# Kernel optimization log

Measured on AMD Instinct MI355X. Metric: run time of the kernel, lower is better.

## Reference

```python
import jax, jax.numpy as jnp
import numpy as np

B, S, D = 8, 1024, 1024   # batch, routed-over rows, feature dim (input_dim)
E = 1024                  # output_dim (== S so gather indices are in range)
K = 2                     # top-k
ALPHA = 0.01


def setup_inputs() -> dict:
    key = jax.random.key(0)
    kx, kw = jax.random.split(key)
    x = jax.random.normal(kx, (B, S, D), dtype=jnp.float32)
    # nn.Linear(input_dim, output_dim, bias=False) weight: [E, D]
    W = jax.random.normal(kw, (E, D), dtype=jnp.float32) / np.sqrt(D).astype(np.float32)
    return {"x": x, "W": W}


def reference(x, W):
    # logits = proj(x): [B, S, E]  (temperature == 1.0 -> no scaling)
    logits = jnp.einsum('bsd,ed->bse', x, W)
    probs = jax.nn.softmax(logits, axis=-1)
    topk_probs, topk_idx = jax.lax.top_k(probs, K)            # [B, S, K]
    # router_selections: gather rows of x along dim 1 -> [B, S, K, D]
    sel = x[jnp.arange(B)[:, None, None], topk_idx]
    # y = sum_k topk_probs * selected rows -> [B, S, D]
    y = jnp.einsum('bsk,bskd->bsd', topk_probs, sel)
    # auxiliary load-balance loss
    router_probs = probs.mean(axis=(0, 1))                    # [E]
    counts = jnp.bincount(topk_idx.reshape(-1), length=E).astype(probs.dtype)
    router_fraction = counts / counts.sum()
    aux_loss = ALPHA * E * jnp.sum(router_probs * router_fraction)
    return y, aux_loss
```

## Files before the change

kernel.cpp:

```cpp
#include <hip/hip_runtime.h>

#define MTOK 8192
#define ED   1024

typedef short s16x8 __attribute__((ext_vector_type(8)));
typedef float f32x4 __attribute__((ext_vector_type(4)));
typedef int   i32x4 __attribute__((ext_vector_type(4)));
typedef unsigned short u16x4 __attribute__((ext_vector_type(4)));

__device__ __forceinline__ unsigned short f2bf(float f) {
    unsigned u = __builtin_bit_cast(unsigned, f);
    u += 0x7fff + ((u >> 16) & 1);
    return (unsigned short)(u >> 16);
}
__device__ __forceinline__ float bf2f(unsigned short h) {
    unsigned u = ((unsigned)h) << 16;
    return __builtin_bit_cast(float, u);
}

__global__ __launch_bounds__(256) void split_bf16_kernel(
        const float* __restrict__ src, unsigned short* __restrict__ hi,
        unsigned short* __restrict__ lo, int* __restrict__ counts, int n4) {
    if (blockIdx.x == 0) {
#pragma unroll
        for (int i = 0; i < 4; ++i) counts[threadIdx.x + i * 256] = 0;
    }
    int idx = blockIdx.x * 256 + threadIdx.x;
    const int stride = gridDim.x * 256;
    for (; idx < n4; idx += stride) {
        float4 v = ((const float4*)src)[idx];
        u16x4 h, l;
        h[0] = f2bf(v.x); l[0] = f2bf(v.x - bf2f(h[0]));
        h[1] = f2bf(v.y); l[1] = f2bf(v.y - bf2f(h[1]));
        h[2] = f2bf(v.z); l[2] = f2bf(v.z - bf2f(h[2]));
        h[3] = f2bf(v.w); l[3] = f2bf(v.w - bf2f(h[3]));
        ((u16x4*)hi)[idx] = h;
        ((u16x4*)lo)[idx] = l;
    }
}

__device__ __forceinline__ void gload16(const void* g, void* l) {
    __builtin_amdgcn_global_load_lds(
        (const __attribute__((address_space(1))) void*)g,
        (__attribute__((address_space(3))) void*)l, 16, 0, 0);
}

__device__ __forceinline__ int cvtpk(float a, float b) {
    int r;
    asm("v_cvt_pk_bf16_f32 %0, %1, %2" : "=v"(r) : "v"(a), "v"(b));
    return r;
}

__device__ __forceinline__ void cvt_write(void* dstHi, void* dstLo,
                                          const float4 f0, const float4 f1) {
    i32x4 h, l;
    h[0] = cvtpk(f0.x, f0.y); h[1] = cvtpk(f0.z, f0.w);
    h[2] = cvtpk(f1.x, f1.y); h[3] = cvtpk(f1.z, f1.w);
    l[0] = cvtpk(f0.x - __builtin_bit_cast(float, h[0] << 16),
                 f0.y - __builtin_bit_cast(float, h[0] & 0xffff0000));
    l[1] = cvtpk(f0.z - __builtin_bit_cast(float, h[1] << 16),
                 f0.w - __builtin_bit_cast(float, h[1] & 0xffff0000));
    l[2] = cvtpk(f1.x - __builtin_bit_cast(float, h[2] << 16),
                 f1.y - __builtin_bit_cast(float, h[2] & 0xffff0000));
    l[3] = cvtpk(f1.z - __builtin_bit_cast(float, h[3] << 16),
                 f1.w - __builtin_bit_cast(float, h[3] & 0xffff0000));
    *(i32x4*)dstHi = h;
    *(i32x4*)dstLo = l;
}

__global__ __launch_bounds__(256, 2) void gemm_mfma_split_kernel(
        const float* __restrict__ Xf,
        const unsigned short* __restrict__ Whi, const unsigned short* __restrict__ Wlo,
        float* __restrict__ C) {
    __shared__ __align__(16) unsigned char smem[2 * 32768];

    const int bid = blockIdx.x;
    const int xcd = bid & 7;
    const int j   = bid >> 3;
    const int bm  = xcd * 8 + (j >> 3);
    const int bn  = j & 7;

    const int tid  = threadIdx.x;
    const int lane = tid & 63;
    const int wid  = tid >> 6;

    const int srow = lane >> 2;
    const int sg   = (lane & 3) ^ ((lane >> 3) & 3);
    const float* gA = Xf + (size_t)(bm * 128 + wid * 32 + srow) * ED + sg * 8;
    const unsigned short* gB = ((wid < 2) ? Whi : Wlo)
            + (size_t)(bn * 128 + (wid & 1) * 64 + srow) * ED + sg * 8;
    unsigned char* const dB = smem + 16384 + ((wid < 2) ? 0 : 8192) + (wid & 1) * 4096;

    float4 fA0, fA1, fA2, fA3;

#define ALOAD(kk)                                                    \
    fA0 = *(const float4*)(gA + (kk));                               \
    fA1 = *(const float4*)(gA + (kk) + 4);                           \
    fA2 = *(const float4*)(gA + (kk) + 16 * 1024);                   \
    fA3 = *(const float4*)(gA + (kk) + 16 * 1024 + 4);

#define BSTAGE(buf, kk)                                              \
    _Pragma("unroll")                                                \
    for (int c = 0; c < 4; ++c)                                      \
        gload16(gB + (kk) + c * (16 * ED), dB + (buf) * 32768 + c * 1024);

#define AWRITE(buf)                                                              \
    cvt_write(smem + (buf) * 32768 + (2 * wid) * 1024 + lane * 16,               \
              smem + (buf) * 32768 + 8192 + (2 * wid) * 1024 + lane * 16,        \
              fA0, fA1);                                                         \
    cvt_write(smem + (buf) * 32768 + (2 * wid + 1) * 1024 + lane * 16,           \
              smem + (buf) * 32768 + 8192 + (2 * wid + 1) * 1024 + lane * 16,    \
              fA2, fA3);

    const int wm = wid >> 1, wn = wid & 1;
    const int fr = lane & 15, fg = lane >> 4;
    const int pg = fg ^ ((fr >> 1) & 3);
    const int aoff = (wm * 64 + fr) * 32 + pg * 8;
    const int boff = (wn * 64 + fr) * 32 + pg * 8;

    f32x4 acc[4][4] = {};

    ALOAD(0);
    BSTAGE(0, 0);
    AWRITE(0);
    asm volatile("s_waitcnt vmcnt(0) lgkmcnt(0)" ::: "memory");
    __builtin_amdgcn_s_barrier();

    for (int t = 0; t < 32; ++t) {
        const int cur = t & 1;
        if (t < 31) { ALOAD((t + 1) * 32); BSTAGE(cur ^ 1, (t + 1) * 32); }

        const unsigned short* Ah = (const unsigned short*)(smem + cur * 32768);
        const unsigned short* Al = Ah + 4096;
        const unsigned short* Bh = Ah + 8192;
        const unsigned short* Bl = Ah + 12288;

        s16x8 ah[4], al[4], bh[4], bl[4];
#pragma unroll
        for (int i = 0; i < 4; ++i) {
            ah[i] = *(const s16x8*)&Ah[aoff + i * 512];
            al[i] = *(const s16x8*)&Al[aoff + i * 512];
            bh[i] = *(const s16x8*)&Bh[boff + i * 512];
            bl[i] = *(const s16x8*)&Bl[boff + i * 512];
        }
#pragma unroll
        for (int i = 0; i < 4; ++i)
#pragma unroll
            for (int jj = 0; jj < 4; ++jj) {
                acc[i][jj] = __builtin_amdgcn_mfma_f32_16x16x32_bf16(ah[i], bh[jj], acc[i][jj], 0, 0, 0);
                acc[i][jj] = __builtin_amdgcn_mfma_f32_16x16x32_bf16(ah[i], bl[jj], acc[i][jj], 0, 0, 0);
                acc[i][jj] = __builtin_amdgcn_mfma_f32_16x16x32_bf16(al[i], bh[jj], acc[i][jj], 0, 0, 0);
            }

        if (t < 31) AWRITE(cur ^ 1);

        asm volatile("s_waitcnt vmcnt(0) lgkmcnt(0)" ::: "memory");
        __builtin_amdgcn_s_barrier();
    }
#undef ALOAD
#undef BSTAGE
#undef AWRITE

    const int crow = bm * 128 + wm * 64 + fg * 4;
    const int ccol = bn * 128 + wn * 64 + fr;
#pragma unroll
    for (int i = 0; i < 4; ++i)
#pragma unroll
        for (int jj = 0; jj < 4; ++jj)
#pragma unroll
            for (int r = 0; r < 4; ++r)
                C[(size_t)(crow + i * 16 + r) * ED + ccol + jj * 16] = acc[i][jj][r];
}

#define BM 128
#define BN 128
#define BK 32
#define LDA (BM + 4)
#define LDB (BN + 4)

__global__ __launch_bounds__(256) void gemm_logits_kernel(const float* __restrict__ X,
                                                          const float* __restrict__ W,
                                                          float* __restrict__ C) {
    __shared__ float As[BK][LDA];
    __shared__ float Bs[BK][LDB];
    const int bm  = blockIdx.y * BM;
    const int bn  = blockIdx.x * BN;
    const int tid = threadIdx.x;
    const int tx  = tid & 15;
    const int ty  = tid >> 4;
    const int lr  = tid >> 3;
    const int lc  = (tid & 7) << 2;

    float acc[8][8];
#pragma unroll
    for (int i = 0; i < 8; ++i)
#pragma unroll
        for (int j = 0; j < 8; ++j) acc[i][j] = 0.f;

    for (int k0 = 0; k0 < ED; k0 += BK) {
#pragma unroll
        for (int i = 0; i < 4; ++i) {
            const int r = lr + i * 32;
            float4 va = *(const float4*)&X[(size_t)(bm + r) * ED + k0 + lc];
            As[lc + 0][r] = va.x; As[lc + 1][r] = va.y;
            As[lc + 2][r] = va.z; As[lc + 3][r] = va.w;
            float4 vb = *(const float4*)&W[(size_t)(bn + r) * ED + k0 + lc];
            Bs[lc + 0][r] = vb.x; Bs[lc + 1][r] = vb.y;
            Bs[lc + 2][r] = vb.z; Bs[lc + 3][r] = vb.w;
        }
        __syncthreads();
#pragma unroll
        for (int kk = 0; kk < BK; ++kk) {
            float a[8], b[8];
            *(float4*)&a[0] = *(const float4*)&As[kk][ty * 8];
            *(float4*)&a[4] = *(const float4*)&As[kk][ty * 8 + 4];
            *(float4*)&b[0] = *(const float4*)&Bs[kk][tx * 8];
            *(float4*)&b[4] = *(const float4*)&Bs[kk][tx * 8 + 4];
#pragma unroll
            for (int i = 0; i < 8; ++i)
#pragma unroll
                for (int j = 0; j < 8; ++j)
                    acc[i][j] = fmaf(a[i], b[j], acc[i][j]);
        }
        __syncthreads();
    }
#pragma unroll
    for (int i = 0; i < 8; ++i) {
        const int r = bm + ty * 8 + i;
        float4* dst = (float4*)&C[(size_t)r * ED + bn + tx * 8];
        dst[0] = make_float4(acc[i][0], acc[i][1], acc[i][2], acc[i][3]);
        dst[1] = make_float4(acc[i][4], acc[i][5], acc[i][6], acc[i][7]);
    }
}

__device__ __forceinline__ bool better(float v, int i, float bv, int bi) {
    return (v > bv) || (v == bv && i < bi);
}

__global__ __launch_bounds__(256, 8) void softmax_wave_kernel(
        const float* __restrict__ X, float* __restrict__ OUT,
        float* __restrict__ partial, int* __restrict__ counts) {
    __shared__ float L[4 * 1024];
    const int tid  = threadIdx.x;
    const int lane = tid & 63;
    const int w    = tid >> 6;
    const int t    = blockIdx.x * 4 + w;

    const float4* row4 = (const float4*)&OUT[(size_t)t * ED];
    float4 p[4];
#pragma unroll
    for (int i = 0; i < 4; ++i) p[i] = row4[lane + 64 * i];

    float v1 = -1e30f, v2 = -1e30f; int i1 = 0x7fffffff, i2 = 0x7fffffff;
#pragma unroll
    for (int i = 0; i < 4; ++i) {
        const float vv[4] = {p[i].x, p[i].y, p[i].z, p[i].w};
#pragma unroll
        for (int c = 0; c < 4; ++c) {
            const int e = 256 * i + 4 * lane + c;
            const float v = vv[c];
            if (better(v, e, v1, i1)) { v2 = v1; i2 = i1; v1 = v; i1 = e; }
            else if (better(v, e, v2, i2)) { v2 = v; i2 = e; }
        }
    }
#pragma unroll
    for (int off = 32; off; off >>= 1) {
        const float ov1 = __shfl_xor(v1, off); const int oi1 = __shfl_xor(i1, off);
        const float ov2 = __shfl_xor(v2, off); const int oi2 = __shfl_xor(i2, off);
        if (better(ov1, oi1, v1, i1)) {
            float nv2; int ni2;
            if (better(v1, i1, ov2, oi2)) { nv2 = v1; ni2 = i1; }
            else { nv2 = ov2; ni2 = oi2; }
            v1 = ov1; i1 = oi1; v2 = nv2; i2 = ni2;
        } else if (better(ov1, oi1, v2, i2)) { v2 = ov1; i2 = oi1; }
    }
    const float m = v1;

    float s = 0.f;
#pragma unroll
    for (int i = 0; i < 4; ++i) {
        p[i].x = __expf(p[i].x - m); p[i].y = __expf(p[i].y - m);
        p[i].z = __expf(p[i].z - m); p[i].w = __expf(p[i].w - m);
        s += p[i].x + p[i].y + p[i].z + p[i].w;
    }
#pragma unroll
    for (int off = 32; off; off >>= 1) s += __shfl_xor(s, off);
    const float inv = 1.f / s;

#pragma unroll
    for (int i = 0; i < 4; ++i) {
        float4 q = make_float4(p[i].x * inv, p[i].y * inv, p[i].z * inv, p[i].w * inv);
        *(float4*)&L[w * 1024 + i * 256 + lane * 4] = q;
    }

    const float p1 = inv;
    const float p2 = __expf(v2 - m) * inv;
    const int b = t >> 10;
    const float4* x1 = (const float4*)&X[((size_t)(b << 10) + i1) * ED];
    const float4* x2 = (const float4*)&X[((size_t)(b << 10) + i2) * ED];
    float4* yrow = (float4*)&OUT[(size_t)t * ED];
#pragma unroll
    for (int i = 0; i < 4; ++i) {
        const int idx = lane + 64 * i;
        const float4 a = x1[idx];
        const float4 c = x2[idx];
        float4 r;
        r.x = fmaf(p1, a.x, p2 * c.x);
        r.y = fmaf(p1, a.y, p2 * c.y);
        r.z = fmaf(p1, a.z, p2 * c.z);
        r.w = fmaf(p1, a.w, p2 * c.w);
        yrow[idx] = r;
    }

    if (lane == 0) { atomicAdd(&counts[i1], 1); atomicAdd(&counts[i2], 1); }

    __syncthreads();
    float4 s0 = *(float4*)&L[0 * 1024 + tid * 4];
    float4 s1 = *(float4*)&L[1 * 1024 + tid * 4];
    float4 s2 = *(float4*)&L[2 * 1024 + tid * 4];
    float4 s3 = *(float4*)&L[3 * 1024 + tid * 4];
    float4 r;
    r.x = (s0.x + s1.x) + (s2.x + s3.x);
    r.y = (s0.y + s1.y) + (s2.y + s3.y);
    r.z = (s0.z + s1.z) + (s2.z + s3.z);
    r.w = (s0.w + s1.w) + (s2.w + s3.w);
    *(float4*)&partial[(size_t)blockIdx.x * 1024 + tid * 4] = r;
}

__global__ __launch_bounds__(256) void aux1_kernel(const float* __restrict__ partial,
                                                   const int* __restrict__ counts,
                                                   float* __restrict__ dotPartial) {
    __shared__ float red[16][16];
    const int tid = threadIdx.x;
    const int el  = tid & 15;
    const int ch  = tid >> 4;
    const int e   = blockIdx.x * 16 + el;
    float s = 0.f;
    for (int k = 0; k < 128; ++k)
        s += partial[(size_t)(ch * 128 + k) * 1024 + e];
    red[ch][el] = s;
    __syncthreads();
    if (tid < 16) {
        float rs = 0.f;
#pragma unroll
        for (int c = 0; c < 16; ++c) rs += red[c][tid];
        float val = rs * (float)counts[blockIdx.x * 16 + tid];
#pragma unroll
        for (int off = 8; off; off >>= 1) val += __shfl_xor(val, off);
        if (tid == 0) dotPartial[blockIdx.x] = val;
    }
}

__global__ void aux2_kernel(const float* __restrict__ dotPartial, float* __restrict__ out) {
    const int lane = threadIdx.x;
    float v = dotPartial[lane];
#pragma unroll
    for (int off = 32; off; off >>= 1) v += __shfl_xor(v, off);
    if (lane == 0)
        out[(size_t)MTOK * ED] = v * (0.01f * 1024.f / (8192.f * 16384.f));
}

#define TOKS_PER_BLK 16
__global__ __launch_bounds__(256) void softmax_topk_y_kernel(
        const float* __restrict__ X, float* __restrict__ OUT,
        float* __restrict__ router_sum, int* __restrict__ counts) {
    __shared__ float routerLocal[ED];
    __shared__ float redMax[4];
    __shared__ float redSum[4];
    __shared__ float wV1[4]; __shared__ int wI1[4];
    __shared__ float wV2[4]; __shared__ int wI2[4];

    const int tid  = threadIdx.x;
    const int lane = tid & 63;
    const int wave = tid >> 6;

    for (int e = tid; e < ED; e += 256) routerLocal[e] = 0.f;
    __syncthreads();

    const int t0 = blockIdx.x * TOKS_PER_BLK;
    for (int t = t0; t < t0 + TOKS_PER_BLK; ++t) {
        const float* lrow = &OUT[(size_t)t * ED];
        float l[4];
#pragma unroll
        for (int i = 0; i < 4; ++i) l[i] = lrow[tid + i * 256];

        float m = fmaxf(fmaxf(l[0], l[1]), fmaxf(l[2], l[3]));
#pragma unroll
        for (int off = 32; off; off >>= 1) m = fmaxf(m, __shfl_xor(m, off));
        if (lane == 0) redMax[wave] = m;
        __syncthreads();
        m = fmaxf(fmaxf(redMax[0], redMax[1]), fmaxf(redMax[2], redMax[3]));

        float p[4]; float s = 0.f;
#pragma unroll
        for (int i = 0; i < 4; ++i) { p[i] = expf(l[i] - m); s += p[i]; }
#pragma unroll
        for (int off = 32; off; off >>= 1) s += __shfl_xor(s, off);
        if (lane == 0) redSum[wave] = s;

        float v1 = -1e30f, v2 = -1e30f; int i1 = 0x7fffffff, i2 = 0x7fffffff;
#pragma unroll
        for (int i = 0; i < 4; ++i) {
            const float v = l[i]; const int ix = tid + i * 256;
            if (better(v, ix, v1, i1)) { v2 = v1; i2 = i1; v1 = v; i1 = ix; }
            else if (better(v, ix, v2, i2)) { v2 = v; i2 = ix; }
        }
#pragma unroll
        for (int off = 32; off; off >>= 1) {
            const float ov1 = __shfl_xor(v1, off); const int oi1 = __shfl_xor(i1, off);
            const float ov2 = __shfl_xor(v2, off); const int oi2 = __shfl_xor(i2, off);
            if (better(ov1, oi1, v1, i1)) {
                float nv2; int ni2;
                if (better(v1, i1, ov2, oi2)) { nv2 = v1; ni2 = i1; }
                else { nv2 = ov2; ni2 = oi2; }
                v1 = ov1; i1 = oi1; v2 = nv2; i2 = ni2;
            } else if (better(ov1, oi1, v2, i2)) { v2 = ov1; i2 = oi1; }
        }
        if (lane == 0) { wV1[wave] = v1; wI1[wave] = i1; wV2[wave] = v2; wI2[wave] = i2; }
        __syncthreads();

        v1 = wV1[0]; i1 = wI1[0]; v2 = wV2[0]; i2 = wI2[0];
#pragma unroll
        for (int w = 1; w < 4; ++w) {
            const float ov1 = wV1[w]; const int oi1 = wI1[w];
            const float ov2 = wV2[w]; const int oi2 = wI2[w];
            if (better(ov1, oi1, v1, i1)) {
                float nv2; int ni2;
                if (better(v1, i1, ov2, oi2)) { nv2 = v1; ni2 = i1; }
                else { nv2 = ov2; ni2 = oi2; }
                v1 = ov1; i1 = oi1; v2 = nv2; i2 = ni2;
            } else if (better(ov1, oi1, v2, i2)) { v2 = ov1; i2 = oi1; }
        }
        const float stot = redSum[0] + redSum[1] + redSum[2] + redSum[3];
        const float inv = 1.f / stot;

#pragma unroll
        for (int i = 0; i < 4; ++i) routerLocal[tid + i * 256] += p[i] * inv;

        const float p1 = expf(v1 - m) * inv;
        const float p2 = expf(v2 - m) * inv;

        const int b = t >> 10;
        const float4* x1 = (const float4*)&X[((size_t)(b << 10) + i1) * ED];
        const float4* x2 = (const float4*)&X[((size_t)(b << 10) + i2) * ED];
        float4* yrow = (float4*)&OUT[(size_t)t * ED];
        const float4 a = x1[tid];
        const float4 c = x2[tid];
        float4 r;
        r.x = fmaf(p1, a.x, p2 * c.x);
        r.y = fmaf(p1, a.y, p2 * c.y);
        r.z = fmaf(p1, a.z, p2 * c.z);
        r.w = fmaf(p1, a.w, p2 * c.w);
        yrow[tid] = r;

        if (tid == 0) { atomicAdd(&counts[i1], 1); atomicAdd(&counts[i2], 1); }
        __syncthreads();
    }

    for (int e = tid; e < ED; e += 256) atomicAdd(&router_sum[e], routerLocal[e]);
}

__global__ __launch_bounds__(256) void aux_kernel(const float* __restrict__ router_sum,
                                                  const int* __restrict__ counts,
                                                  float* __restrict__ out) {
    __shared__ float red[4];
    const int tid = threadIdx.x;
    float s = 0.f;
    for (int e = tid; e < ED; e += 256)
        s += (router_sum[e] * (1.f / 8192.f)) * ((float)counts[e] * (1.f / 16384.f));
#pragma unroll
    for (int off = 32; off; off >>= 1) s += __shfl_xor(s, off);
    if ((tid & 63) == 0) red[tid >> 6] = s;
    __syncthreads();
    if (tid == 0) out[(size_t)MTOK * ED] = 0.01f * 1024.f * (red[0] + red[1] + red[2] + red[3]);
}

extern "C" void kernel_launch(void* const* d_in, const int* in_sizes, int n_in,
                              void* d_out, int out_size, void* d_ws, size_t ws_size,
                              hipStream_t stream) {
    const float* X = (const float*)d_in[0];
    const float* W = (const float*)d_in[1];
    float* out = (float*)d_out;

    const size_t WS_NEED = (size_t)ED * ED * 2 * sizeof(unsigned short)
                         + (size_t)2048 * 1024 * sizeof(float)
                         + 64 * sizeof(float) + ED * sizeof(int);

    if (ws_size >= WS_NEED) {
        unsigned short* Whi = (unsigned short*)d_ws;
        unsigned short* Wlo = Whi + (size_t)ED * ED;
        float* partial      = (float*)(Wlo + (size_t)ED * ED);
        float* dotPartial   = partial + (size_t)2048 * 1024;
        int*   counts       = (int*)(dotPartial + 64);

        split_bf16_kernel<<<512, 256, 0, stream>>>(W, Whi, Wlo, counts, ED * ED / 4);
        gemm_mfma_split_kernel<<<512, 256, 0, stream>>>(X, Whi, Wlo, out);
        softmax_wave_kernel<<<MTOK / 4, 256, 0, stream>>>(X, out, partial, counts);
        aux1_kernel<<<64, 256, 0, stream>>>(partial, counts, dotPartial);
        aux2_kernel<<<1, 64, 0, stream>>>(dotPartial, out);
    } else {
        float* router_sum = (float*)d_ws;
        int*   counts     = (int*)((char*)d_ws + ED * sizeof(float));
        hipMemsetAsync(d_ws, 0, ED * (sizeof(float) + sizeof(int)), stream);
        dim3 ggrid(ED / BN, MTOK / BM);
        gemm_logits_kernel<<<ggrid, 256, 0, stream>>>(X, W, out);
        softmax_topk_y_kernel<<<MTOK / TOKS_PER_BLK, 256, 0, stream>>>(X, out, router_sum, counts);
        aux_kernel<<<1, 256, 0, stream>>>(router_sum, counts, out);
    }
}
```

Before: 90.69 us.

## Load X fragments directly into MFMA registers, shrink GEMM tile to 128x64

Rewrites the split-bf16 MFMA GEMM so each wave loads its fp32 X rows straight from global memory in MFMA fragment layout and converts them to hi/lo bf16 in registers, with no staging through LDS. Only the W hi/lo tiles go through LDS. The block tile shrinks from 128x128 to 128x64, with each wave owning 32 rows, and the grid doubles to 1024 blocks with occupancy raised to 4 blocks per CU. The aim is to remove the LDS write/read traffic for A and raise occupancy. The cost is that the X tile is reloaded by twice as many column blocks and there is less reuse per block.

```diff
diff --git a/kernel.cpp b/kernel.cpp
--- a/kernel.cpp
+++ b/kernel.cpp
@@ -51,8 +51,8 @@
     return r;
 }
 
-__device__ __forceinline__ void cvt_write(void* dstHi, void* dstLo,
-                                          const float4 f0, const float4 f1) {
+__device__ __forceinline__ void cvt_regs(const float4 f0, const float4 f1,
+                                         s16x8* hi, s16x8* lo) {
     i32x4 h, l;
     h[0] = cvtpk(f0.x, f0.y); h[1] = cvtpk(f0.z, f0.w);
     h[2] = cvtpk(f1.x, f1.y); h[3] = cvtpk(f1.z, f1.w);
@@ -64,112 +64,101 @@
                  f1.y - __builtin_bit_cast(float, h[2] & 0xffff0000));
     l[3] = cvtpk(f1.z - __builtin_bit_cast(float, h[3] << 16),
                  f1.w - __builtin_bit_cast(float, h[3] & 0xffff0000));
-    *(i32x4*)dstHi = h;
-    *(i32x4*)dstLo = l;
-}
-
-__global__ __launch_bounds__(256, 2) void gemm_mfma_split_kernel(
+    *hi = __builtin_bit_cast(s16x8, h);
+    *lo = __builtin_bit_cast(s16x8, l);
+}
+
+__global__ __launch_bounds__(256, 4) void gemm_direct_kernel(
         const float* __restrict__ Xf,
         const unsigned short* __restrict__ Whi, const unsigned short* __restrict__ Wlo,
         float* __restrict__ C) {
-    __shared__ __align__(16) unsigned char smem[2 * 32768];
+    __shared__ __align__(16) unsigned char smem[2 * 8192];
 
     const int bid = blockIdx.x;
     const int xcd = bid & 7;
     const int j   = bid >> 3;
-    const int bm  = xcd * 8 + (j >> 3);
-    const int bn  = j & 7;
-
-    const int tid  = threadIdx.x;
-    const int lane = tid & 63;
-    const int wid  = tid >> 6;
+    const int bm  = xcd * 8 + (j >> 4);
+    const int bn  = j & 15;
+
+    const int lane = threadIdx.x & 63;
+    const int wid  = threadIdx.x >> 6;
+    const int fr = lane & 15, fg = lane >> 4;
+    const int pg = fg ^ ((fr >> 1) & 3);
+
+    const float* gA = Xf + (size_t)(bm * 128 + wid * 32 + fr) * ED + fg * 8;
 
     const int srow = lane >> 2;
     const int sg   = (lane & 3) ^ ((lane >> 3) & 3);
-    const float* gA = Xf + (size_t)(bm * 128 + wid * 32 + srow) * ED + sg * 8;
     const unsigned short* gB = ((wid < 2) ? Whi : Wlo)
-            + (size_t)(bn * 128 + (wid & 1) * 64 + srow) * ED + sg * 8;
-    unsigned char* const dB = smem + 16384 + ((wid < 2) ? 0 : 8192) + (wid & 1) * 4096;
-
-    float4 fA0, fA1, fA2, fA3;
-
-#define ALOAD(kk)                                                    \
-    fA0 = *(const float4*)(gA + (kk));                               \
-    fA1 = *(const float4*)(gA + (kk) + 4);                           \
-    fA2 = *(const float4*)(gA + (kk) + 16 * 1024);                   \
-    fA3 = *(const float4*)(gA + (kk) + 16 * 1024 + 4);
-
-#define BSTAGE(buf, kk)                                              \
-    _Pragma("unroll")                                                \
-    for (int c = 0; c < 4; ++c)                                      \
-        gload16(gB + (kk) + c * (16 * ED), dB + (buf) * 32768 + c * 1024);
-
-#define AWRITE(buf)                                                              \
-    cvt_write(smem + (buf) * 32768 + (2 * wid) * 1024 + lane * 16,               \
-              smem + (buf) * 32768 + 8192 + (2 * wid) * 1024 + lane * 16,        \
-              fA0, fA1);                                                         \
-    cvt_write(smem + (buf) * 32768 + (2 * wid + 1) * 1024 + lane * 16,           \
-              smem + (buf) * 32768 + 8192 + (2 * wid + 1) * 1024 + lane * 16,    \
-              fA2, fA3);
-
-    const int wm = wid >> 1, wn = wid & 1;
-    const int fr = lane & 15, fg = lane >> 4;
-    const int pg = fg ^ ((fr >> 1) & 3);
-    const int aoff = (wm * 64 + fr) * 32 + pg * 8;
-    const int boff = (wn * 64 + fr) * 32 + pg * 8;
-
-    f32x4 acc[4][4] = {};
-
-    ALOAD(0);
+            + (size_t)(bn * 64 + (wid & 1) * 32 + srow) * ED + sg * 8;
+    unsigned char* const dB = smem + ((wid < 2) ? 0 : 4096) + (wid & 1) * 2048;
+
+#define BSTAGE(buf, kk)                                                  \
+    _Pragma("unroll")                                                    \
+    for (int c = 0; c < 2; ++c)                                          \
+        gload16(gB + (kk) + c * (16 * ED), dB + (buf) * 8192 + c * 1024);
+
+#define ALOAD(S, T)                                                      \
+    fA##S[0] = *(const float4*)(gA + (T) * 32);                          \
+    fA##S[1] = *(const float4*)(gA + (T) * 32 + 4);                      \
+    fA##S[2] = *(const float4*)(gA + (size_t)16 * ED + (T) * 32);        \
+    fA##S[3] = *(const float4*)(gA + (size_t)16 * ED + (T) * 32 + 4);
+
+#define CVT(S)                                                           \
+    cvt_regs(fA##S[0], fA##S[1], &ah[0], &al[0]);                        \
+    cvt_regs(fA##S[2], fA##S[3], &ah[1], &al[1]);
+
+#define COMPUTE(BUF)                                                     \
+    _Pragma("unroll")                                                    \
+    for (int cb = 0; cb < 4; ++cb) {                                     \
+        const int off = (BUF) * 8192 + cb * 1024 + fr * 64 + pg * 16;    \
+        const s16x8 bh = *(const s16x8*)(smem + off);                    \
+        const s16x8 bl = *(const s16x8*)(smem + 4096 + off);             \
+        _Pragma("unroll")                                                \
+        for (int rb = 0; rb < 2; ++rb) {                                 \
+            acc[rb][cb] = __builtin_amdgcn_mfma_f32_16x16x32_bf16(ah[rb], bh, acc[rb][cb], 0, 0, 0); \
+            acc[rb][cb] = __builtin_amdgcn_mfma_f32_16x16x32_bf16(ah[rb], bl, acc[rb][cb], 0, 0, 0); \
+            acc[rb][cb] = __builtin_amdgcn_mfma_f32_16x16x32_bf16(al[rb], bh, acc[rb][cb], 0, 0, 0); \
+        }                                                                \
+    }
+
+#define STEP(T, SCUR, SNXT, BUF)                                         \
+    {                                                                    \
+        CVT(SCUR);                                                       \
+        if ((T) < 31) { ALOAD(SNXT, (T) + 1); BSTAGE((BUF) ^ 1, ((T) + 1) * 32); } \
+        COMPUTE(BUF);                                                    \
+        asm volatile("s_waitcnt vmcnt(0) lgkmcnt(0)" ::: "memory");      \
+        __builtin_amdgcn_s_barrier();                                    \
+    }
+
+    float4 fA0[4], fA1[4];
+    s16x8 ah[2], al[2];
+    f32x4 acc[2][4] = {};
+
+    ALOAD(0, 0);
     BSTAGE(0, 0);
-    AWRITE(0);
-    asm volatile("s_waitcnt vmcnt(0) lgkmcnt(0)" ::: "memory");
+    asm volatile("s_waitcnt vmcnt(0)" ::: "memory");
     __builtin_amdgcn_s_barrier();
 
-    for (int t = 0; t < 32; ++t) {
-        const int cur = t & 1;
-        if (t < 31) { ALOAD((t + 1) * 32); BSTAGE(cur ^ 1, (t + 1) * 32); }
-
-        const unsigned short* Ah = (const unsigned short*)(smem + cur * 32768);
-        const unsigned short* Al = Ah + 4096;
-        const unsigned short* Bh = Ah + 8192;
-        const unsigned short* Bl = Ah + 12288;
-
-        s16x8 ah[4], al[4], bh[4], bl[4];
-#pragma unroll
-        for (int i = 0; i < 4; ++i) {
-            ah[i] = *(const s16x8*)&Ah[aoff + i * 512];
-            al[i] = *(const s16x8*)&Al[aoff + i * 512];
-            bh[i] = *(const s16x8*)&Bh[boff + i * 512];
-            bl[i] = *(const s16x8*)&Bl[boff + i * 512];
-        }
-#pragma unroll
-        for (int i = 0; i < 4; ++i)
-#pragma unroll
-            for (int jj = 0; jj < 4; ++jj) {
-                acc[i][jj] = __builtin_amdgcn_mfma_f32_16x16x32_bf16(ah[i], bh[jj], acc[i][jj], 0, 0, 0);
-                acc[i][jj] = __builtin_amdgcn_mfma_f32_16x16x32_bf16(ah[i], bl[jj], acc[i][jj], 0, 0, 0);
-                acc[i][jj] = __builtin_amdgcn_mfma_f32_16x16x32_bf16(al[i], bh[jj], acc[i][jj], 0, 0, 0);
-            }
-
-        if (t < 31) AWRITE(cur ^ 1);
-
-        asm volatile("s_waitcnt vmcnt(0) lgkmcnt(0)" ::: "memory");
-        __builtin_amdgcn_s_barrier();
-    }
+    for (int t2 = 0; t2 < 32; t2 += 2) {
+        STEP(t2,     0, 1, 0)
+        STEP(t2 + 1, 1, 0, 1)
+    }
+#undef STEP
+#undef COMPUTE
+#undef CVT
 #undef ALOAD
 #undef BSTAGE
-#undef AWRITE
-
-    const int crow = bm * 128 + wm * 64 + fg * 4;
-    const int ccol = bn * 128 + wn * 64 + fr;
-#pragma unroll
-    for (int i = 0; i < 4; ++i)
-#pragma unroll
-        for (int jj = 0; jj < 4; ++jj)
+
+    const int crow = bm * 128 + wid * 32 + fg * 4;
+    const int ccol = bn * 64 + fr;
+#pragma unroll
+    for (int rb = 0; rb < 2; ++rb)
+#pragma unroll
+        for (int cb = 0; cb < 4; ++cb)
 #pragma unroll
             for (int r = 0; r < 4; ++r)
-                C[(size_t)(crow + i * 16 + r) * ED + ccol + jj * 16] = acc[i][jj][r];
+                C[(size_t)(crow + rb * 16 + r) * ED + ccol + cb * 16] = acc[rb][cb][r];
 }
 
 #define BM 128
@@ -494,7 +483,7 @@
         int*   counts       = (int*)(dotPartial + 64);
 
         split_bf16_kernel<<<512, 256, 0, stream>>>(W, Whi, Wlo, counts, ED * ED / 4);
-        gemm_mfma_split_kernel<<<512, 256, 0, stream>>>(X, Whi, Wlo, out);
+        gemm_direct_kernel<<<1024, 256, 0, stream>>>(X, Whi, Wlo, out);
         softmax_wave_kernel<<<MTOK / 4, 256, 0, stream>>>(X, out, partial, counts);
         aux1_kernel<<<64, 256, 0, stream>>>(partial, counts, dotPartial);
         aux2_kernel<<<1, 64, 0, stream>>>(dotPartial, out);
```

Result: slower. 114.6 us (+26.4%).
